# Optimization experiments

Measured on AMD Instinct MI355X. Metric: run time of the kernel, lower is better.

## Reference

```python
import jax, jax.numpy as jnp
import numpy as np

N = 50000          # total_nodes (B*N diagonal-stacked graphs)
E = 800000         # total edges (avg degree 16)
HID = 128          # hidden_size
HEADS = 8          # num_heads


def setup_inputs() -> dict:
    key = jax.random.key(0)
    ks = jax.random.split(key, 10)
    s = 1.0 / np.sqrt(HID)
    x = jax.random.normal(ks[0], (N, HID), jnp.float32)
    edge_index = jax.random.randint(ks[1], (2, E), 0, N, dtype=jnp.int32).astype(jnp.int64)
    Wq = jax.random.normal(ks[2], (HID, HID), jnp.float32) * s
    bq = jax.random.normal(ks[3], (HID,), jnp.float32) * 0.01
    Wk = jax.random.normal(ks[4], (HID, HID), jnp.float32) * s
    bk = jax.random.normal(ks[5], (HID,), jnp.float32) * 0.01
    Wv = jax.random.normal(ks[6], (HID, HID), jnp.float32) * s
    bv = jax.random.normal(ks[7], (HID,), jnp.float32) * 0.01
    Wo = jax.random.normal(ks[8], (HID, HID), jnp.float32) * s
    bo = jax.random.normal(ks[9], (HID,), jnp.float32) * 0.01
    return {"x": x, "edge_index": edge_index, "total_nodes": N,
            "Wq": Wq, "bq": bq, "Wk": Wk, "bk": bk,
            "Wv": Wv, "bv": bv, "Wo": Wo, "bo": bo}


def reference(x, edge_index, total_nodes, Wq, bq, Wk, bk, Wv, bv, Wo, bo):
    H = HEADS
    D = HID // HEADS
    scale = D ** (-0.5)
    # torch Linear: y = x @ W.T + b
    Q = (x @ Wq.T + bq).reshape(-1, H, D)   # (N, H, D)
    K = (x @ Wk.T + bk).reshape(-1, H, D)
    V = (x @ Wv.T + bv).reshape(-1, H, D)
    src = edge_index[0]
    dst = edge_index[1]
    # edge-wise dot-product scores: (E, H)
    scores = jnp.einsum('ehd,ehd->eh', Q[dst], K[src]) * scale
    # scatter-softmax over edges sharing the same dst node
    mx = jax.ops.segment_max(scores, dst, num_segments=total_nodes)      # (N, H)
    ex = jnp.exp(scores - mx[dst])                                        # (E, H)
    se = jax.ops.segment_sum(ex, dst, num_segments=total_nodes)          # (N, H)
    attn = ex / (se[dst] + 1e-12)                                         # (E, H)
    # weighted message aggregation
    msg = attn[..., None] * V[src]                                        # (E, H, D)
    out = jax.ops.segment_sum(msg, dst, num_segments=total_nodes)        # (N, H, D)
    out = out.reshape(total_nodes, HID)
    return out @ Wo.T + bo
```

## Files before the change

kernel.cpp:

```cpp
#include <hip/hip_runtime.h>
#include <math.h>

#define NNODES 50000
#define NEDGES 800000
#define HIDDEN 128
#define NH 8
#define CAP 64
#define NPART 8
#define PART_SZ 6250
#define SCAT_BPP 128
#define SCAT_BLOCKS (NPART * SCAT_BPP)
#define QKV_WAVES 1563
#define QKV_BLOCKS 391

typedef __bf16 bf16x8 __attribute__((ext_vector_type(8)));
typedef float  f32x4  __attribute__((ext_vector_type(4)));

__device__ inline unsigned short f2b(float f) {
    unsigned u = __float_as_uint(f);
    unsigned r = (u + 0x7fffu + ((u >> 16) & 1u)) >> 16;
    return (unsigned short)r;
}

__device__ inline bf16x8 ld_a8(const float* __restrict__ p) {
    float4 a = *(const float4*)p;
    float4 b = *(const float4*)(p + 4);
    bf16x8 r;
    r[0] = (__bf16)a.x; r[1] = (__bf16)a.y; r[2] = (__bf16)a.z; r[3] = (__bf16)a.w;
    r[4] = (__bf16)b.x; r[5] = (__bf16)b.y; r[6] = (__bf16)b.z; r[7] = (__bf16)b.w;
    return r;
}

__global__ __launch_bounds__(256)
void pack_init(const float* __restrict__ Wq, const float* __restrict__ Wk,
               const float* __restrict__ Wv, const float* __restrict__ Wo,
               unsigned short* __restrict__ Pqkv, unsigned short* __restrict__ Po,
               int* __restrict__ cnt)
{
    if (blockIdx.x >= 32) {
        const int idx = (blockIdx.x - 32) * 256 + threadIdx.x;
        if (idx < NNODES / 4) ((int4*)cnt)[idx] = make_int4(0, 0, 0, 0);
        return;
    }
    const int s = blockIdx.x * 4 + (threadIdx.x >> 6);
    const int lane = threadIdx.x & 63;
    const float* W; unsigned short* P; int ct, c;
    if (s < 96) { ct = s >> 2; c = s & 3;
        W = (ct < 8) ? Wq : (ct < 16) ? Wk : Wv;
        P = Pqkv + (size_t)s * 512;
        ct &= 7;
    } else { int t = s - 96; ct = t >> 2; c = t & 3; W = Wo; P = Po + (size_t)t * 512; }
    const int colin = ct * 16 + (lane & 15);
    const int k0 = c * 32 + (lane >> 4) * 8;
    const float* sp = W + (size_t)colin * 128 + k0;
    unsigned short v[8];
#pragma unroll
    for (int j = 0; j < 8; ++j) v[j] = f2b(sp[j]);
    uint4 o;
    o.x = (unsigned)v[0] | ((unsigned)v[1] << 16);
    o.y = (unsigned)v[2] | ((unsigned)v[3] << 16);
    o.z = (unsigned)v[4] | ((unsigned)v[5] << 16);
    o.w = (unsigned)v[6] | ((unsigned)v[7] << 16);
    *(uint4*)(P + lane * 8) = o;
}

__global__ __launch_bounds__(256)
void qkv_scatter(const float* __restrict__ x, const unsigned short* __restrict__ Pqkv,
                 const float* __restrict__ bq, const float* __restrict__ bk,
                 const float* __restrict__ bv,
                 const int* __restrict__ src, const int* __restrict__ dst,
                 unsigned short* __restrict__ Qb, unsigned short* __restrict__ KVb,
                 int* __restrict__ cnt, int* __restrict__ bucket)
{
    if (blockIdx.x >= QKV_BLOCKS) {
        const int sb = blockIdx.x - QKV_BLOCKS;
        const int part = sb & (NPART - 1);
        const int blk  = sb >> 3;
        const int lo = part * PART_SZ, hi = lo + PART_SZ;
        for (int e = blk * 256 + threadIdx.x; e < NEDGES; e += SCAT_BPP * 256) {
            const int d = dst[e];
            if (d >= lo && d < hi) {
                const int pos = atomicAdd(&cnt[d], 1);
                if (pos < CAP) bucket[d * CAP + pos] = src[e];
            }
        }
        return;
    }

    const int w = blockIdx.x * 4 + (threadIdx.x >> 6);
    if (w >= QKV_WAVES) return;
    const int lane = threadIdx.x & 63;
    const int row0 = w * 32;
    const int ar = lane & 15, kg = lane >> 4;
    const bool two = (row0 + 16) < NNODES;

    const float* ap0 = x + (size_t)(row0 + ar) * 128 + kg * 8;
    const float* ap1 = two ? (ap0 + 16 * 128) : ap0;
    const bf16x8 a00 = ld_a8(ap0), a01 = ld_a8(ap0 + 32), a02 = ld_a8(ap0 + 64), a03 = ld_a8(ap0 + 96);
    const bf16x8 a10 = ld_a8(ap1), a11 = ld_a8(ap1 + 32), a12 = ld_a8(ap1 + 64), a13 = ld_a8(ap1 + 96);

    const unsigned short* wp = Pqkv + lane * 8;
    bf16x8 nb0 = *(const bf16x8*)(wp);
    bf16x8 nb1 = *(const bf16x8*)(wp + 512);
    bf16x8 nb2 = *(const bf16x8*)(wp + 1024);
    bf16x8 nb3 = *(const bf16x8*)(wp + 1536);

#pragma unroll
    for (int t = 0; t < 24; ++t) {
        const bf16x8 b0 = nb0, b1 = nb1, b2 = nb2, b3 = nb3;
        if (t < 23) {
            const unsigned short* nw = wp + (size_t)(t + 1) * 2048;
            nb0 = *(const bf16x8*)(nw);
            nb1 = *(const bf16x8*)(nw + 512);
            nb2 = *(const bf16x8*)(nw + 1024);
            nb3 = *(const bf16x8*)(nw + 1536);
        }
        f32x4 acc0 = {0.f, 0.f, 0.f, 0.f};
        f32x4 acc1 = {0.f, 0.f, 0.f, 0.f};
        acc0 = __builtin_amdgcn_mfma_f32_16x16x32_bf16(a00, b0, acc0, 0, 0, 0);
        acc1 = __builtin_amdgcn_mfma_f32_16x16x32_bf16(a10, b0, acc1, 0, 0, 0);
        acc0 = __builtin_amdgcn_mfma_f32_16x16x32_bf16(a01, b1, acc0, 0, 0, 0);
        acc1 = __builtin_amdgcn_mfma_f32_16x16x32_bf16(a11, b1, acc1, 0, 0, 0);
        acc0 = __builtin_amdgcn_mfma_f32_16x16x32_bf16(a02, b2, acc0, 0, 0, 0);
        acc1 = __builtin_amdgcn_mfma_f32_16x16x32_bf16(a12, b2, acc1, 0, 0, 0);
        acc0 = __builtin_amdgcn_mfma_f32_16x16x32_bf16(a03, b3, acc0, 0, 0, 0);
        acc1 = __builtin_amdgcn_mfma_f32_16x16x32_bf16(a13, b3, acc1, 0, 0, 0);

        const int sel = t >> 3;
        const int colin = (t & 7) * 16 + ar;
        if (sel == 0) {
            const float bsc = bq[colin];
#pragma unroll
            for (int j = 0; j < 4; ++j)
                Qb[(size_t)(row0 + kg * 4 + j) * 128 + colin] = f2b(acc0[j] + bsc);
            if (two) {
#pragma unroll
                for (int j = 0; j < 4; ++j)
                    Qb[(size_t)(row0 + 16 + kg * 4 + j) * 128 + colin] = f2b(acc1[j] + bsc);
            }
        } else {
            const float bsc = (sel == 1) ? bk[colin] : bv[colin];
            const int cbase = (colin >> 1) * 4 + (colin & 1) + ((sel == 2) ? 2 : 0);
#pragma unroll
            for (int j = 0; j < 4; ++j)
                KVb[(size_t)(row0 + kg * 4 + j) * 256 + cbase] = f2b(acc0[j] + bsc);
            if (two) {
#pragma unroll
                for (int j = 0; j < 4; ++j)
                    KVb[(size_t)(row0 + 16 + kg * 4 + j) * 256 + cbase] = f2b(acc1[j] + bsc);
            }
        }
    }
}

__global__ __launch_bounds__(256)
void fused_attn_kernel(const unsigned short* __restrict__ Qb,
                       const unsigned short* __restrict__ KVb,
                       const int* __restrict__ cnt, const int* __restrict__ bucket,
                       unsigned short* __restrict__ accumb)
{
    const int wave = threadIdx.x >> 6;
    const int lane = threadIdx.x & 63;
    const int n = blockIdx.x * 4 + wave;
    if (n >= NNODES) return;

    int deg = cnt[n];
    deg = deg > CAP ? CAP : deg;
    const int mysrc = (lane < deg) ? bucket[n * CAP + lane] : 0;

    const unsigned short* kvbase = KVb + lane * 4;

    const unsigned qw = *(const unsigned*)(Qb + (size_t)n * HIDDEN + lane * 2);
    const float qx = __uint_as_float(qw << 16) * 0.25f;
    const float qy = __uint_as_float(qw & 0xffff0000u) * 0.25f;

    float m = -INFINITY, s = 0.f, ox = 0.f, oy = 0.f;

    uint2 kvA = make_uint2(0,0), kvB = kvA, kvC = kvA, kvD = kvA;
    if (deg > 0) kvA = *(const uint2*)(kvbase + ((size_t)__shfl(mysrc, 0) << 8));
    if (deg > 1) kvB = *(const uint2*)(kvbase + ((size_t)__shfl(mysrc, 1) << 8));
    if (deg > 2) kvC = *(const uint2*)(kvbase + ((size_t)__shfl(mysrc, 2) << 8));
    if (deg > 3) kvD = *(const uint2*)(kvbase + ((size_t)__shfl(mysrc, 3) << 8));

    int i = 0;
    for (; i + 2 <= deg; i += 2) {
        const uint2 c0 = kvA, c1 = kvB;
        kvA = kvC; kvB = kvD;
        if (i + 4 < deg) kvC = *(const uint2*)(kvbase + ((size_t)__shfl(mysrc, i + 4) << 8));
        if (i + 5 < deg) kvD = *(const uint2*)(kvbase + ((size_t)__shfl(mysrc, i + 5) << 8));

        float d0 = qx * __uint_as_float(c0.x << 16) + qy * __uint_as_float(c0.x & 0xffff0000u);
        float d1 = qx * __uint_as_float(c1.x << 16) + qy * __uint_as_float(c1.x & 0xffff0000u);
        d0 += __shfl_xor(d0, 1);  d1 += __shfl_xor(d1, 1);
        d0 += __shfl_xor(d0, 2);  d1 += __shfl_xor(d1, 2);
        d0 += __shfl_xor(d0, 4);  d1 += __shfl_xor(d1, 4);

        const float pm = fmaxf(d0, d1);
        const float ee = __expf(-fabsf(d0 - d1));
        const bool g = d0 >= d1;
        const float v0x = __uint_as_float(c0.y << 16), v0y = __uint_as_float(c0.y & 0xffff0000u);
        const float v1x = __uint_as_float(c1.y << 16), v1y = __uint_as_float(c1.y & 0xffff0000u);
        const float sp  = 1.f + ee;
        const float ovx = fmaf(ee, g ? v1x : v0x, g ? v0x : v1x);
        const float ovy = fmaf(ee, g ? v1y : v0y, g ? v0y : v1y);

        const float dd = pm - m;
        const float em = __expf(-fabsf(dd));
        const bool nm = dd > 0.f;
        const float so = nm ? em : 1.f;
        const float sn = nm ? 1.f : em;
        m = nm ? pm : m;
        s  = fmaf(s,  so, sp  * sn);
        ox = fmaf(ox, so, ovx * sn);
        oy = fmaf(oy, so, ovy * sn);
    }
    if (i < deg) {
        const uint2 c0 = kvA;
        float d0 = qx * __uint_as_float(c0.x << 16) + qy * __uint_as_float(c0.x & 0xffff0000u);
        d0 += __shfl_xor(d0, 1);
        d0 += __shfl_xor(d0, 2);
        d0 += __shfl_xor(d0, 4);
        const float vx = __uint_as_float(c0.y << 16), vy = __uint_as_float(c0.y & 0xffff0000u);
        const float dd = d0 - m;
        const float em = __expf(-fabsf(dd));
        const bool nm = dd > 0.f;
        const float so = nm ? em : 1.f;
        const float pp = nm ? 1.f : em;
        m = nm ? d0 : m;
        s  = fmaf(s,  so, pp);
        ox = fmaf(ox, so, pp * vx);
        oy = fmaf(oy, so, pp * vy);
    }
    const float inv = 1.f / (s + 1e-12f);
    ushort2 ob = { f2b(ox * inv), f2b(oy * inv) };
    *(ushort2*)(accumb + (size_t)n * HIDDEN + lane * 2) = ob;
}

__global__ __launch_bounds__(256)
void outproj_mfma(const unsigned short* __restrict__ accumb, const unsigned short* __restrict__ Po,
                  const float* __restrict__ bo, float* __restrict__ out)
{
    const int band = blockIdx.x * 4 + (threadIdx.x >> 6);
    if (band >= 3125) return;
    const int lane = threadIdx.x & 63;
    const int row0 = band * 16;
    const int ar = lane & 15, kg = lane >> 4;

    const unsigned short* ab = accumb + (size_t)(row0 + ar) * 128 + kg * 8;
    const bf16x8 a0 = *(const bf16x8*)(ab);
    const bf16x8 a1 = *(const bf16x8*)(ab + 32);
    const bf16x8 a2 = *(const bf16x8*)(ab + 64);
    const bf16x8 a3 = *(const bf16x8*)(ab + 96);

    const unsigned short* wp = Po + lane * 8;
    bf16x8 pb0 = *(const bf16x8*)(wp);
    bf16x8 pb1 = *(const bf16x8*)(wp + 512);
    bf16x8 pb2 = *(const bf16x8*)(wp + 1024);
    bf16x8 pb3 = *(const bf16x8*)(wp + 1536);

#pragma unroll
    for (int t = 0; t < 8; ++t) {
        const bf16x8 b0 = pb0, b1 = pb1, b2 = pb2, b3 = pb3;
        if (t < 7) {
            const unsigned short* nw = wp + (size_t)(t + 1) * 2048;
            pb0 = *(const bf16x8*)(nw);
            pb1 = *(const bf16x8*)(nw + 512);
            pb2 = *(const bf16x8*)(nw + 1024);
            pb3 = *(const bf16x8*)(nw + 1536);
        }
        f32x4 acc = {0.f, 0.f, 0.f, 0.f};
        acc = __builtin_amdgcn_mfma_f32_16x16x32_bf16(a0, b0, acc, 0, 0, 0);
        acc = __builtin_amdgcn_mfma_f32_16x16x32_bf16(a1, b1, acc, 0, 0, 0);
        acc = __builtin_amdgcn_mfma_f32_16x16x32_bf16(a2, b2, acc, 0, 0, 0);
        acc = __builtin_amdgcn_mfma_f32_16x16x32_bf16(a3, b3, acc, 0, 0, 0);

        const int colin = t * 16 + ar;
        const float bsc = bo[colin];
#pragma unroll
        for (int j = 0; j < 4; ++j)
            out[(size_t)(row0 + kg * 4 + j) * 128 + colin] = acc[j] + bsc;
    }
}

extern "C" void kernel_launch(void* const* d_in, const int* in_sizes, int n_in,
                              void* d_out, int out_size, void* d_ws, size_t ws_size,
                              hipStream_t stream) {
    const float* x  = (const float*)d_in[0];
    const int*   ei = (const int*)d_in[1];
    const int*   src = ei;
    const int*   dst = ei + NEDGES;
    const float* Wq = (const float*)d_in[3];
    const float* bq = (const float*)d_in[4];
    const float* Wk = (const float*)d_in[5];
    const float* bk = (const float*)d_in[6];
    const float* Wv = (const float*)d_in[7];
    const float* bv = (const float*)d_in[8];
    const float* Wo = (const float*)d_in[9];
    const float* bo = (const float*)d_in[10];
    float* out = (float*)d_out;

    char* ws = (char*)d_ws;
    size_t off = 0;
    const size_t sz_nhb = (size_t)NNODES * HIDDEN * sizeof(unsigned short);
    unsigned short* Qb     = (unsigned short*)(ws + off); off += sz_nhb;
    unsigned short* KVb    = (unsigned short*)(ws + off); off += 2 * sz_nhb;
    unsigned short* accumb = (unsigned short*)(ws + off); off += sz_nhb;
    unsigned short* Pqkv   = (unsigned short*)(ws + off); off += 96 * 512 * sizeof(unsigned short);
    unsigned short* Po     = (unsigned short*)(ws + off); off += 32 * 512 * sizeof(unsigned short);
    int*            cnt    = (int*)(ws + off);            off += (size_t)NNODES * sizeof(int);
    int*            bucket = (int*)(ws + off);            off += (size_t)NNODES * CAP * sizeof(int);

    pack_init<<<81, 256, 0, stream>>>(Wq, Wk, Wv, Wo, Pqkv, Po, cnt);

    qkv_scatter<<<QKV_BLOCKS + SCAT_BLOCKS, 256, 0, stream>>>(
        x, Pqkv, bq, bk, bv, src, dst, Qb, KVb, cnt, bucket);

    fused_attn_kernel<<<(NNODES + 3) / 4, 256, 0, stream>>>(Qb, KVb, cnt, bucket, accumb);

    outproj_mfma<<<782, 256, 0, stream>>>(accumb, Po, bo, out);
}
```

Measured before the change: 133.6 us.

## Deepen KV prefetch to 8 edges, process 4 per step, stage KV stores via LDS

The attention kernel now keeps eight gathered K/V rows in flight and merges four edges per online-softmax step through a tree combine, aiming to hide gather latency and shorten the dependency chain. The QKV kernel writes K/V results into shared memory first and then copies them out as coalesced 16-byte rows, replacing scattered 2-byte global stores. Blocks shrink to 128 threads, with the grid adjusted so that coverage is unchanged. The cost is more registers per wave in the attention kernel, which may reduce occupancy, and remainder edges now load without prefetch.

```diff
diff --git a/kernel.cpp b/kernel.cpp
--- a/kernel.cpp
+++ b/kernel.cpp
@@ -8,10 +8,9 @@
 #define CAP 64
 #define NPART 8
 #define PART_SZ 6250
-#define SCAT_BPP 128
-#define SCAT_BLOCKS (NPART * SCAT_BPP)
+#define SCAT_BLOCKS 1024
 #define QKV_WAVES 1563
-#define QKV_BLOCKS 391
+#define QKV_BLOCKS 782
 
 typedef __bf16 bf16x8 __attribute__((ext_vector_type(8)));
 typedef float  f32x4  __attribute__((ext_vector_type(4)));
@@ -21,6 +20,8 @@
     unsigned r = (u + 0x7fffu + ((u >> 16) & 1u)) >> 16;
     return (unsigned short)r;
 }
+__device__ inline float bl(unsigned u) { return __uint_as_float(u << 16); }
+__device__ inline float bh(unsigned u) { return __uint_as_float(u & 0xffff0000u); }
 
 __device__ inline bf16x8 ld_a8(const float* __restrict__ p) {
     float4 a = *(const float4*)p;
@@ -64,7 +65,7 @@
     *(uint4*)(P + lane * 8) = o;
 }
 
-__global__ __launch_bounds__(256)
+__global__ __launch_bounds__(128)
 void qkv_scatter(const float* __restrict__ x, const unsigned short* __restrict__ Pqkv,
                  const float* __restrict__ bq, const float* __restrict__ bk,
                  const float* __restrict__ bv,
@@ -72,12 +73,14 @@
                  unsigned short* __restrict__ Qb, unsigned short* __restrict__ KVb,
                  int* __restrict__ cnt, int* __restrict__ bucket)
 {
+    __shared__ __align__(16) unsigned short lkv[2][2][16][264];
+
     if (blockIdx.x >= QKV_BLOCKS) {
         const int sb = blockIdx.x - QKV_BLOCKS;
         const int part = sb & (NPART - 1);
         const int blk  = sb >> 3;
         const int lo = part * PART_SZ, hi = lo + PART_SZ;
-        for (int e = blk * 256 + threadIdx.x; e < NEDGES; e += SCAT_BPP * 256) {
+        for (int e = blk * 128 + threadIdx.x; e < NEDGES; e += 128 * 128) {
             const int d = dst[e];
             if (d >= lo && d < hi) {
                 const int pos = atomicAdd(&cnt[d], 1);
@@ -87,7 +90,8 @@
         return;
     }
 
-    const int w = blockIdx.x * 4 + (threadIdx.x >> 6);
+    const int wv = threadIdx.x >> 6;
+    const int w = blockIdx.x * 2 + wv;
     if (w >= QKV_WAVES) return;
     const int lane = threadIdx.x & 63;
     const int row0 = w * 32;
@@ -143,14 +147,97 @@
             const int cbase = (colin >> 1) * 4 + (colin & 1) + ((sel == 2) ? 2 : 0);
 #pragma unroll
             for (int j = 0; j < 4; ++j)
-                KVb[(size_t)(row0 + kg * 4 + j) * 256 + cbase] = f2b(acc0[j] + bsc);
+                lkv[wv][0][kg * 4 + j][cbase] = f2b(acc0[j] + bsc);
             if (two) {
 #pragma unroll
                 for (int j = 0; j < 4; ++j)
-                    KVb[(size_t)(row0 + 16 + kg * 4 + j) * 256 + cbase] = f2b(acc1[j] + bsc);
+                    lkv[wv][1][kg * 4 + j][cbase] = f2b(acc1[j] + bsc);
             }
         }
     }
+
+#pragma unroll
+    for (int b = 0; b < 2; ++b) {
+        if (b == 1 && !two) break;
+#pragma unroll
+        for (int it = 0; it < 8; ++it) {
+            const int chunk = lane + it * 64;
+            const int r = chunk >> 5, c = chunk & 31;
+            const uint4 v = *(const uint4*)&lkv[wv][b][r][c * 8];
+            *(uint4*)(KVb + (size_t)(row0 + b * 16 + r) * 256 + c * 8) = v;
+        }
+    }
+}
+
+#define LOADKV(slot, idx) do { const int _ix = (idx); \
+    if (_ix < deg) { const int _sd = __shfl(mysrc, _ix); \
+        slot = *(const uint2*)(kvbase + ((size_t)_sd << 8)); } } while (0)
+
+__device__ inline void proc4(const uint2 c0, const uint2 c1, const uint2 c2, const uint2 c3,
+                             const float qx, const float qy,
+                             float& m, float& s, float& ox, float& oy)
+{
+    float d0 = qx * bl(c0.x) + qy * bh(c0.x);
+    float d1 = qx * bl(c1.x) + qy * bh(c1.x);
+    float d2 = qx * bl(c2.x) + qy * bh(c2.x);
+    float d3 = qx * bl(c3.x) + qy * bh(c3.x);
+    d0 += __shfl_xor(d0, 1); d1 += __shfl_xor(d1, 1); d2 += __shfl_xor(d2, 1); d3 += __shfl_xor(d3, 1);
+    d0 += __shfl_xor(d0, 2); d1 += __shfl_xor(d1, 2); d2 += __shfl_xor(d2, 2); d3 += __shfl_xor(d3, 2);
+    d0 += __shfl_xor(d0, 4); d1 += __shfl_xor(d1, 4); d2 += __shfl_xor(d2, 4); d3 += __shfl_xor(d3, 4);
+
+    const float pm01 = fmaxf(d0, d1);
+    const float ee01 = __expf(-fabsf(d0 - d1));
+    const bool  g01  = d0 >= d1;
+    const float sp01 = 1.f + ee01;
+    const float o01x = fmaf(ee01, g01 ? bl(c1.y) : bl(c0.y), g01 ? bl(c0.y) : bl(c1.y));
+    const float o01y = fmaf(ee01, g01 ? bh(c1.y) : bh(c0.y), g01 ? bh(c0.y) : bh(c1.y));
+    const float pm23 = fmaxf(d2, d3);
+    const float ee23 = __expf(-fabsf(d2 - d3));
+    const bool  g23  = d2 >= d3;
+    const float sp23 = 1.f + ee23;
+    const float o23x = fmaf(ee23, g23 ? bl(c3.y) : bl(c2.y), g23 ? bl(c2.y) : bl(c3.y));
+    const float o23y = fmaf(ee23, g23 ? bh(c3.y) : bh(c2.y), g23 ? bh(c2.y) : bh(c3.y));
+    const float pmR = fmaxf(pm01, pm23);
+    const float eeR = __expf(-fabsf(pm01 - pm23));
+    const bool  gR  = pm01 >= pm23;
+    const float sR  = fmaf(eeR, gR ? sp23 : sp01, gR ? sp01 : sp23);
+    const float oRx = fmaf(eeR, gR ? o23x : o01x, gR ? o01x : o23x);
+    const float oRy = fmaf(eeR, gR ? o23y : o01y, gR ? o01y : o23y);
+    const float dd = pmR - m;
+    const float em = __expf(-fabsf(dd));
+    const bool  nm = dd > 0.f;
+    const float so = nm ? em : 1.f;
+    const float sn = nm ? 1.f : em;
+    m  = nm ? pmR : m;
+    s  = fmaf(s,  so, sR  * sn);
+    ox = fmaf(ox, so, oRx * sn);
+    oy = fmaf(oy, so, oRy * sn);
+}
+
+__device__ inline void proc2(const uint2 c0, const uint2 c1,
+                             const float qx, const float qy,
+                             float& m, float& s, float& ox, float& oy)
+{
+    float d0 = qx * bl(c0.x) + qy * bh(c0.x);
+    float d1 = qx * bl(c1.x) + qy * bh(c1.x);
+    d0 += __shfl_xor(d0, 1); d1 += __shfl_xor(d1, 1);
+    d0 += __shfl_xor(d0, 2); d1 += __shfl_xor(d1, 2);
+    d0 += __shfl_xor(d0, 4); d1 += __shfl_xor(d1, 4);
+    const float pm = fmaxf(d0, d1);
+    const float ee = __expf(-fabsf(d0 - d1));
+    const bool  g  = d0 >= d1;
+    const float sp = 1.f + ee;
+    const float ovx = fmaf(ee, g ? bl(c1.y) : bl(c0.y), g ? bl(c0.y) : bl(c1.y));
+    const float ovy = fmaf(ee, g ? bh(c1.y) : bh(c0.y), g ? bh(c0.y) : bh(c1.y));
+    const float dd = pm - m;
+    const float em = __expf(-fabsf(dd));
+    const bool  nm = dd > 0.f;
+    const float so = nm ? em : 1.f;
+    const float sn = nm ? 1.f : em;
+    m  = nm ? pm : m;
+    s  = fmaf(s,  so, sp  * sn);
+    ox = fmaf(ox, so, ovx * sn);
+    oy = fmaf(oy, so, ovy * sn);
 }
 
 __global__ __launch_bounds__(256)
@@ -167,70 +254,54 @@
     int deg = cnt[n];
     deg = deg > CAP ? CAP : deg;
     const int mysrc = (lane < deg) ? bucket[n * CAP + lane] : 0;
-
     const unsigned short* kvbase = KVb + lane * 4;
 
     const unsigned qw = *(const unsigned*)(Qb + (size_t)n * HIDDEN + lane * 2);
-    const float qx = __uint_as_float(qw << 16) * 0.25f;
-    const float qy = __uint_as_float(qw & 0xffff0000u) * 0.25f;
+    const float qx = bl(qw) * 0.25f;
+    const float qy = bh(qw) * 0.25f;
 
     float m = -INFINITY, s = 0.f, ox = 0.f, oy = 0.f;
 
-    uint2 kvA = make_uint2(0,0), kvB = kvA, kvC = kvA, kvD = kvA;
-    if (deg > 0) kvA = *(const uint2*)(kvbase + ((size_t)__shfl(mysrc, 0) << 8));
-    if (deg > 1) kvB = *(const uint2*)(kvbase + ((size_t)__shfl(mysrc, 1) << 8));
-    if (deg > 2) kvC = *(const uint2*)(kvbase + ((size_t)__shfl(mysrc, 2) << 8));
-    if (deg > 3) kvD = *(const uint2*)(kvbase + ((size_t)__shfl(mysrc, 3) << 8));
+    uint2 kv0 = make_uint2(0, 0), kv1 = kv0, kv2 = kv0, kv3 = kv0;
+    uint2 kv4 = kv0, kv5 = kv0, kv6 = kv0, kv7 = kv0;
+    LOADKV(kv0, 0); LOADKV(kv1, 1); LOADKV(kv2, 2); LOADKV(kv3, 3);
+    LOADKV(kv4, 4); LOADKV(kv5, 5); LOADKV(kv6, 6); LOADKV(kv7, 7);
 
     int i = 0;
+    while (true) {
+        if (i + 4 > deg) break;
+        proc4(kv0, kv1, kv2, kv3, qx, qy, m, s, ox, oy);
+        LOADKV(kv0, i + 8); LOADKV(kv1, i + 9); LOADKV(kv2, i + 10); LOADKV(kv3, i + 11);
+        i += 4;
+        if (i + 4 > deg) break;
+        proc4(kv4, kv5, kv6, kv7, qx, qy, m, s, ox, oy);
+        LOADKV(kv4, i + 8); LOADKV(kv5, i + 9); LOADKV(kv6, i + 10); LOADKV(kv7, i + 11);
+        i += 4;
+    }
     for (; i + 2 <= deg; i += 2) {
-        const uint2 c0 = kvA, c1 = kvB;
-        kvA = kvC; kvB = kvD;
-        if (i + 4 < deg) kvC = *(const uint2*)(kvbase + ((size_t)__shfl(mysrc, i + 4) << 8));
-        if (i + 5 < deg) kvD = *(const uint2*)(kvbase + ((size_t)__shfl(mysrc, i + 5) << 8));
-
-        float d0 = qx * __uint_as_float(c0.x << 16) + qy * __uint_as_float(c0.x & 0xffff0000u);
-        float d1 = qx * __uint_as_float(c1.x << 16) + qy * __uint_as_float(c1.x & 0xffff0000u);
-        d0 += __shfl_xor(d0, 1);  d1 += __shfl_xor(d1, 1);
-        d0 += __shfl_xor(d0, 2);  d1 += __shfl_xor(d1, 2);
-        d0 += __shfl_xor(d0, 4);  d1 += __shfl_xor(d1, 4);
-
-        const float pm = fmaxf(d0, d1);
-        const float ee = __expf(-fabsf(d0 - d1));
-        const bool g = d0 >= d1;
-        const float v0x = __uint_as_float(c0.y << 16), v0y = __uint_as_float(c0.y & 0xffff0000u);
-        const float v1x = __uint_as_float(c1.y << 16), v1y = __uint_as_float(c1.y & 0xffff0000u);
-        const float sp  = 1.f + ee;
-        const float ovx = fmaf(ee, g ? v1x : v0x, g ? v0x : v1x);
-        const float ovy = fmaf(ee, g ? v1y : v0y, g ? v0y : v1y);
-
-        const float dd = pm - m;
-        const float em = __expf(-fabsf(dd));
-        const bool nm = dd > 0.f;
-        const float so = nm ? em : 1.f;
-        const float sn = nm ? 1.f : em;
-        m = nm ? pm : m;
-        s  = fmaf(s,  so, sp  * sn);
-        ox = fmaf(ox, so, ovx * sn);
-        oy = fmaf(oy, so, ovy * sn);
+        uint2 c0, c1;
+        { const int sd = __shfl(mysrc, i);     c0 = *(const uint2*)(kvbase + ((size_t)sd << 8)); }
+        { const int sd = __shfl(mysrc, i + 1); c1 = *(const uint2*)(kvbase + ((size_t)sd << 8)); }
+        proc2(c0, c1, qx, qy, m, s, ox, oy);
     }
     if (i < deg) {
-        const uint2 c0 = kvA;
-        float d0 = qx * __uint_as_float(c0.x << 16) + qy * __uint_as_float(c0.x & 0xffff0000u);
+        uint2 c0;
+        { const int sd = __shfl(mysrc, i); c0 = *(const uint2*)(kvbase + ((size_t)sd << 8)); }
+        float d0 = qx * bl(c0.x) + qy * bh(c0.x);
         d0 += __shfl_xor(d0, 1);
         d0 += __shfl_xor(d0, 2);
         d0 += __shfl_xor(d0, 4);
-        const float vx = __uint_as_float(c0.y << 16), vy = __uint_as_float(c0.y & 0xffff0000u);
         const float dd = d0 - m;
         const float em = __expf(-fabsf(dd));
-        const bool nm = dd > 0.f;
+        const bool  nm = dd > 0.f;
         const float so = nm ? em : 1.f;
         const float pp = nm ? 1.f : em;
-        m = nm ? d0 : m;
+        m  = nm ? d0 : m;
         s  = fmaf(s,  so, pp);
-        ox = fmaf(ox, so, pp * vx);
-        oy = fmaf(oy, so, pp * vy);
-    }
+        ox = fmaf(ox, so, pp * bl(c0.y));
+        oy = fmaf(oy, so, pp * bh(c0.y));
+    }
+
     const float inv = 1.f / (s + 1e-12f);
     ushort2 ob = { f2b(ox * inv), f2b(oy * inv) };
     *(ushort2*)(accumb + (size_t)n * HIDDEN + lane * 2) = ob;
@@ -312,7 +383,7 @@
 
     pack_init<<<81, 256, 0, stream>>>(Wq, Wk, Wv, Wo, Pqkv, Po, cnt);
 
-    qkv_scatter<<<QKV_BLOCKS + SCAT_BLOCKS, 256, 0, stream>>>(
+    qkv_scatter<<<QKV_BLOCKS + SCAT_BLOCKS, 128, 0, stream>>>(
         x, Pqkv, bq, bk, bv, src, dst, Qb, KVb, cnt, bucket);
 
     fused_attn_kernel<<<(NNODES + 3) / 4, 256, 0, stream>>>(Qb, KVb, cnt, bucket, accumb);
```

After: 173.6 us. 1.3x slower.
